# Kernel tuning notes

Hardware: AMD Instinct MI355X
Metric: run time of the kernel (lower is better)

Reference implementation:

```python
import jax, jax.numpy as jnp
import numpy as np

B, T = 8192, 2048


def setup_inputs() -> dict:
    key = jax.random.key(0)
    u = jax.random.normal(key, (B, T, 1), dtype=jnp.float32)
    return {
        "u": u,
        "dt": jnp.float32(0.01),
        "m": jnp.float32(1.0),
        "c": jnp.float32(0.1),
        "k": jnp.float32(2.0),
        "in_mean": jnp.float32(0.5),
        "in_std": jnp.float32(2.0),
        "out_mean": jnp.float32(0.0),
        "out_std": jnp.float32(1.5),
    }


def reference(u, dt, m, c, k, in_mean, in_std, out_mean, out_std):
    # u: (B, T, 1) scaled forcing signal; state: (B, 2) = [position, velocity]
    Bsz = u.shape[0]
    u_seq = jnp.transpose(u[..., 0])  # (T, B) for lax.scan over time
    state0 = jnp.zeros((Bsz, 2), dtype=u.dtype)

    def step(state, u_t):
        # in_s.inverse_transform: unscale input
        u_p = u_t * in_std + in_mean  # (B,)
        x, v = state[:, 0], state[:, 1]
        # prior(state, u_p): mass-spring-damper derivative [dx, dv]
        acc = (u_p - c * v - k * x) / m
        new_state = state + dt * jnp.stack([v, acc], axis=1)  # Euler step
        # prior.ay on the UPDATED state (matches torch: state updated first)
        ay = (u_p - c * new_state[:, 1] - k * new_state[:, 0]) / m
        # out_s.transform: scale output
        y = (ay - out_mean) / out_std  # (B,)
        return new_state, y

    state_T, ys = jax.lax.scan(step, state0, u_seq)  # ys: (T, B)
    return jnp.transpose(ys), state_T  # (B, T), (B, 2)
```

## Files before the change

### kernel.cpp

```cpp
#include <hip/hip_runtime.h>

#define TT 2048
#define LP 32
#define RPB 4
#define NR  2
#define ROW_GRAN_PAD 320

typedef unsigned int v4u __attribute__((ext_vector_type(4)));

__device__ __forceinline__ float b2f(unsigned short h) {
    union { unsigned int u; float f; } x; x.u = ((unsigned int)h) << 16; return x.f;
}
__device__ __forceinline__ unsigned short f2b(float f) {
    union { float f; unsigned int u; } x; x.f = f;
    unsigned int r = x.u + 0x7fffu + ((x.u >> 16) & 1u);
    return (unsigned short)(r >> 16);
}
__device__ __forceinline__ float ldsc(const void* p, bool bf) {
    return bf ? b2f(*(const unsigned short*)p) : *(const float*)p;
}

__global__ __launch_bounds__(256, 4) void phys_scan(
    const void* __restrict__ u_in,
    const void* __restrict__ p_dt, const void* __restrict__ p_m,
    const void* __restrict__ p_c,  const void* __restrict__ p_k,
    const void* __restrict__ p_im, const void* __restrict__ p_is,
    const void* __restrict__ p_om, const void* __restrict__ p_os,
    void* __restrict__ out, int rows)
{
    __shared__ v4u smem[RPB * ROW_GRAN_PAD];

    const int lane = threadIdx.x & 63;
    const int w    = threadIdx.x >> 6;
    const int wid  = blockIdx.x * RPB + w;
    if (wid * NR >= rows) return;

    const bool bf = (((const unsigned short*)p_m)[0] != 0);

    const float dt = ldsc(p_dt, bf);
    const float mm = ldsc(p_m,  bf);
    const float cc = ldsc(p_c,  bf);
    const float kk = ldsc(p_k,  bf);
    const float im = ldsc(p_im, bf);
    const float is = ldsc(p_is, bf);
    const float om = ldsc(p_om, bf);
    const float os = ldsc(p_os, bf);

    const float inv_m  = 1.0f / mm;
    const float inv_os = 1.0f / os;
    const float a21 = -dt * kk * inv_m;
    const float a22 = 1.0f - dt * cc * inv_m;
    const float dtm = dt * inv_m;

    v4u* lrow = &smem[w * ROW_GRAN_PAD];

    if (bf) {
        const unsigned short* ub = (const unsigned short*)u_in;
        unsigned short*       ob = (unsigned short*)out;

        v4u st[NR][4];
        #pragma unroll
        for (int rr = 0; rr < NR; ++rr) {
            const v4u* g = (const v4u*)(ub + (size_t)(wid * NR + rr) * TT);
            #pragma unroll
            for (int it = 0; it < 4; ++it)
                st[rr][it] = __builtin_nontemporal_load(&g[it * 64 + lane]);
        }

        #pragma unroll
        for (int rr = 0; rr < NR; ++rr) {
            const int b = wid * NR + rr;

            #pragma unroll
            for (int it = 0; it < 4; ++it) {
                int p = it * 64 + lane;
                lrow[p + (p >> 2)] = st[rr][it];
            }

            float uf[LP];
            #pragma unroll
            for (int j = 0; j < 4; ++j) {
                v4u g = lrow[5 * lane + j];
                unsigned int ws[4] = {g.x, g.y, g.z, g.w};
                #pragma unroll
                for (int q = 0; q < 4; ++q) {
                    uf[j*8 + q*2 + 0] = b2f((unsigned short)(ws[q] & 0xffffu));
                    uf[j*8 + q*2 + 1] = b2f((unsigned short)(ws[q] >> 16));
                }
            }

            float px = 0.f, pv = 0.f;
            #pragma unroll
            for (int i = 0; i < LP; i++) {
                float up = uf[i] * is + im;
                uf[i] = up;
                float nx = px + dt * pv;
                float nv = a21 * px + a22 * pv + dtm * up;
                px = nx; pv = nv;
            }

            float m00 = 1.f, m01 = dt, m10 = a21, m11 = a22;
            #pragma unroll
            for (int i = 0; i < 5; i++) {
                float t00 = m00*m00 + m01*m10;
                float t01 = m00*m01 + m01*m11;
                float t10 = m10*m00 + m11*m10;
                float t11 = m10*m01 + m11*m11;
                m00=t00; m01=t01; m10=t10; m11=t11;
            }

            #pragma unroll
            for (int o = 1; o < 64; o <<= 1) {
                float rx = __shfl_up(px, o, 64);
                float rv = __shfl_up(pv, o, 64);
                if (lane >= o) {
                    px = m00*rx + m01*rv + px;
                    pv = m10*rx + m11*rv + pv;
                }
                if (o < 32) {
                    float t00 = m00*m00 + m01*m10;
                    float t01 = m00*m01 + m01*m11;
                    float t10 = m10*m00 + m11*m10;
                    float t11 = m10*m01 + m11*m11;
                    m00=t00; m01=t01; m10=t10; m11=t11;
                }
            }

            float ex = __shfl_up(px, 1, 64);
            float ev = __shfl_up(pv, 1, 64);
            if (lane == 0) { ex = 0.f; ev = 0.f; }

            float x = ex, v = ev;
            #pragma unroll
            for (int i = 0; i < LP; i++) {
                float up = uf[i];
                float nx = x + dt * v;
                float nv = a21 * x + a22 * v + dtm * up;
                float ay = (up - cc * nv - kk * nx) * inv_m;
                uf[i] = (ay - om) * inv_os;
                x = nx; v = nv;
            }

            #pragma unroll
            for (int j = 0; j < 4; ++j) {
                v4u g;
                g.x = (unsigned)f2b(uf[j*8+0]) | ((unsigned)f2b(uf[j*8+1]) << 16);
                g.y = (unsigned)f2b(uf[j*8+2]) | ((unsigned)f2b(uf[j*8+3]) << 16);
                g.z = (unsigned)f2b(uf[j*8+4]) | ((unsigned)f2b(uf[j*8+5]) << 16);
                g.w = (unsigned)f2b(uf[j*8+6]) | ((unsigned)f2b(uf[j*8+7]) << 16);
                lrow[5 * lane + j] = g;
            }
            v4u* gout = (v4u*)(ob + (size_t)b * TT);
            #pragma unroll
            for (int it = 0; it < 4; ++it) {
                int p = it * 64 + lane;
                gout[p] = lrow[p + (p >> 2)];
            }
            if (lane == 63) {
                size_t so = (size_t)rows * TT + (size_t)b * 2;
                ob[so]   = f2b(px);
                ob[so+1] = f2b(pv);
            }
        }
    } else {
        for (int rr = 0; rr < NR; ++rr) {
            const int b = wid * NR + rr;
            if (b >= rows) break;
            const size_t base = (size_t)b * TT + (size_t)lane * LP;
            float uf[LP];
            const float4* p = (const float4*)((const float*)u_in + base);
            #pragma unroll
            for (int i = 0; i < 8; i++) {
                float4 v4 = p[i];
                uf[i*4+0]=v4.x; uf[i*4+1]=v4.y; uf[i*4+2]=v4.z; uf[i*4+3]=v4.w;
            }
            float px = 0.f, pv = 0.f;
            #pragma unroll
            for (int i = 0; i < LP; i++) {
                float up = uf[i] * is + im;
                uf[i] = up;
                float nx = px + dt * pv;
                float nv = a21 * px + a22 * pv + dtm * up;
                px = nx; pv = nv;
            }
            float m00 = 1.f, m01 = dt, m10 = a21, m11 = a22;
            #pragma unroll
            for (int i = 0; i < 5; i++) {
                float t00 = m00*m00 + m01*m10;
                float t01 = m00*m01 + m01*m11;
                float t10 = m10*m00 + m11*m10;
                float t11 = m10*m01 + m11*m11;
                m00=t00; m01=t01; m10=t10; m11=t11;
            }
            #pragma unroll
            for (int o = 1; o < 64; o <<= 1) {
                float rx = __shfl_up(px, o, 64);
                float rv = __shfl_up(pv, o, 64);
                if (lane >= o) {
                    px = m00*rx + m01*rv + px;
                    pv = m10*rx + m11*rv + pv;
                }
                if (o < 32) {
                    float t00 = m00*m00 + m01*m10;
                    float t01 = m00*m01 + m01*m11;
                    float t10 = m10*m00 + m11*m10;
                    float t11 = m10*m01 + m11*m11;
                    m00=t00; m01=t01; m10=t10; m11=t11;
                }
            }
            float ex = __shfl_up(px, 1, 64);
            float ev = __shfl_up(pv, 1, 64);
            if (lane == 0) { ex = 0.f; ev = 0.f; }
            float x = ex, v = ev;
            #pragma unroll
            for (int i = 0; i < LP; i++) {
                float up = uf[i];
                float nx = x + dt * v;
                float nv = a21 * x + a22 * v + dtm * up;
                float ay = (up - cc * nv - kk * nx) * inv_m;
                uf[i] = (ay - om) * inv_os;
                x = nx; v = nv;
            }
            float* of = (float*)out;
            float4* po = (float4*)(of + base);
            #pragma unroll
            for (int i = 0; i < 8; i++)
                po[i] = make_float4(uf[i*4+0], uf[i*4+1], uf[i*4+2], uf[i*4+3]);
            if (lane == 63) {
                size_t so = (size_t)rows * TT + (size_t)b * 2;
                of[so]   = px;
                of[so+1] = pv;
            }
        }
    }
}

extern "C" void kernel_launch(void* const* d_in, const int* in_sizes, int n_in,
                              void* d_out, int out_size, void* d_ws, size_t ws_size,
                              hipStream_t stream) {
    const int rows = in_sizes[0] / TT;
    const int waves = (rows + NR - 1) / NR;
    const int blocks = (waves + RPB - 1) / RPB;
    hipLaunchKernelGGL(phys_scan, dim3(blocks), dim3(256), 0, stream,
                       d_in[0], d_in[1], d_in[2], d_in[3], d_in[4],
                       d_in[5], d_in[6], d_in[7], d_in[8],
                       d_out, rows);
}
```

Baseline: 145.8 us.

## Drop LDS staging, load rows directly per lane, prefetch next row

The bf16 path no longer stages each row through shared memory. Instead every lane reads its own contiguous 64-byte chunk straight from global memory and writes results back the same way with nontemporal stores. The next row is prefetched while the current one is computed, and float-to-bf16 packing now uses the HIP paired conversion intrinsic. This removes the LDS round trips and barriers-free shuffles, but global accesses become strided per lane, with 64-byte chunks per lane instead of fully coalesced 16-byte-per-lane sweeps.

```diff
diff --git a/kernel.cpp b/kernel.cpp
--- a/kernel.cpp
+++ b/kernel.cpp
@@ -1,23 +1,22 @@
 #include <hip/hip_runtime.h>
+#include <hip/hip_bf16.h>
 
 #define TT 2048
 #define LP 32
 #define RPB 4
 #define NR  2
-#define ROW_GRAN_PAD 320
 
 typedef unsigned int v4u __attribute__((ext_vector_type(4)));
 
 __device__ __forceinline__ float b2f(unsigned short h) {
     union { unsigned int u; float f; } x; x.u = ((unsigned int)h) << 16; return x.f;
 }
-__device__ __forceinline__ unsigned short f2b(float f) {
-    union { float f; unsigned int u; } x; x.f = f;
-    unsigned int r = x.u + 0x7fffu + ((x.u >> 16) & 1u);
-    return (unsigned short)(r >> 16);
-}
 __device__ __forceinline__ float ldsc(const void* p, bool bf) {
     return bf ? b2f(*(const unsigned short*)p) : *(const float*)p;
+}
+__device__ __forceinline__ unsigned int pk2(float a, float b) {
+    __hip_bfloat162 h = __float22bfloat162_rn(float2{a, b});
+    union { __hip_bfloat162 h; unsigned int u; } c; c.h = h; return c.u;
 }
 
 __global__ __launch_bounds__(256, 4) void phys_scan(
@@ -28,8 +27,6 @@
     const void* __restrict__ p_om, const void* __restrict__ p_os,
     void* __restrict__ out, int rows)
 {
-    __shared__ v4u smem[RPB * ROW_GRAN_PAD];
-
     const int lane = threadIdx.x & 63;
     const int w    = threadIdx.x >> 6;
     const int wid  = blockIdx.x * RPB + w;
@@ -52,36 +49,32 @@
     const float a22 = 1.0f - dt * cc * inv_m;
     const float dtm = dt * inv_m;
 
-    v4u* lrow = &smem[w * ROW_GRAN_PAD];
-
     if (bf) {
         const unsigned short* ub = (const unsigned short*)u_in;
         unsigned short*       ob = (unsigned short*)out;
 
-        v4u st[NR][4];
-        #pragma unroll
-        for (int rr = 0; rr < NR; ++rr) {
-            const v4u* g = (const v4u*)(ub + (size_t)(wid * NR + rr) * TT);
-            #pragma unroll
-            for (int it = 0; it < 4; ++it)
-                st[rr][it] = __builtin_nontemporal_load(&g[it * 64 + lane]);
+        v4u cur[4];
+        {
+            const v4u* g = (const v4u*)(ub + (size_t)(wid * NR) * TT) + lane * 4;
+            #pragma unroll
+            for (int j = 0; j < 4; ++j) cur[j] = g[j];
         }
 
         #pragma unroll
         for (int rr = 0; rr < NR; ++rr) {
             const int b = wid * NR + rr;
 
-            #pragma unroll
-            for (int it = 0; it < 4; ++it) {
-                int p = it * 64 + lane;
-                lrow[p + (p >> 2)] = st[rr][it];
+            v4u nxt[4];
+            if (rr + 1 < NR) {
+                const v4u* g = (const v4u*)(ub + (size_t)(b + 1) * TT) + lane * 4;
+                #pragma unroll
+                for (int j = 0; j < 4; ++j) nxt[j] = g[j];
             }
 
             float uf[LP];
             #pragma unroll
             for (int j = 0; j < 4; ++j) {
-                v4u g = lrow[5 * lane + j];
-                unsigned int ws[4] = {g.x, g.y, g.z, g.w};
+                unsigned int ws[4] = {cur[j].x, cur[j].y, cur[j].z, cur[j].w};
                 #pragma unroll
                 for (int q = 0; q < 4; ++q) {
                     uf[j*8 + q*2 + 0] = b2f((unsigned short)(ws[q] & 0xffffu));
@@ -130,37 +123,41 @@
             float ev = __shfl_up(pv, 1, 64);
             if (lane == 0) { ex = 0.f; ev = 0.f; }
 
-            float x = ex, v = ev;
-            #pragma unroll
-            for (int i = 0; i < LP; i++) {
-                float up = uf[i];
-                float nx = x + dt * v;
-                float nv = a21 * x + a22 * v + dtm * up;
-                float ay = (up - cc * nv - kk * nx) * inv_m;
-                uf[i] = (ay - om) * inv_os;
-                x = nx; v = nv;
-            }
-
+            unsigned int yw[16];
+            {
+                float x = ex, v = ev;
+                #pragma unroll
+                for (int i = 0; i < LP; i += 2) {
+                    float up0 = uf[i];
+                    float nx0 = x + dt * v;
+                    float nv0 = a21 * x + a22 * v + dtm * up0;
+                    float y0  = ((up0 - cc * nv0 - kk * nx0) * inv_m - om) * inv_os;
+                    float up1 = uf[i+1];
+                    float nx1 = nx0 + dt * nv0;
+                    float nv1 = a21 * nx0 + a22 * nv0 + dtm * up1;
+                    float y1  = ((up1 - cc * nv1 - kk * nx1) * inv_m - om) * inv_os;
+                    yw[i >> 1] = pk2(y0, y1);
+                    x = nx1; v = nv1;
+                }
+            }
+
+            v4u* go = (v4u*)(ob + (size_t)b * TT) + lane * 4;
             #pragma unroll
             for (int j = 0; j < 4; ++j) {
                 v4u g;
-                g.x = (unsigned)f2b(uf[j*8+0]) | ((unsigned)f2b(uf[j*8+1]) << 16);
-                g.y = (unsigned)f2b(uf[j*8+2]) | ((unsigned)f2b(uf[j*8+3]) << 16);
-                g.z = (unsigned)f2b(uf[j*8+4]) | ((unsigned)f2b(uf[j*8+5]) << 16);
-                g.w = (unsigned)f2b(uf[j*8+6]) | ((unsigned)f2b(uf[j*8+7]) << 16);
-                lrow[5 * lane + j] = g;
-            }
-            v4u* gout = (v4u*)(ob + (size_t)b * TT);
-            #pragma unroll
-            for (int it = 0; it < 4; ++it) {
-                int p = it * 64 + lane;
-                gout[p] = lrow[p + (p >> 2)];
+                g.x = yw[j*4+0]; g.y = yw[j*4+1];
+                g.z = yw[j*4+2]; g.w = yw[j*4+3];
+                __builtin_nontemporal_store(g, &go[j]);
             }
             if (lane == 63) {
                 size_t so = (size_t)rows * TT + (size_t)b * 2;
-                ob[so]   = f2b(px);
-                ob[so+1] = f2b(pv);
-            }
+                unsigned int pk = pk2(px, pv);
+                ob[so]   = (unsigned short)(pk & 0xffffu);
+                ob[so+1] = (unsigned short)(pk >> 16);
+            }
+
+            #pragma unroll
+            for (int j = 0; j < 4; ++j) cur[j] = nxt[j];
         }
     } else {
         for (int rr = 0; rr < NR; ++rr) {
```

After: 152.3 us. 4.4% more time.
